# Kernel tuning notes

Hardware: AMD Instinct MI355X
Metric: run time of the kernel (lower is better)

Reference implementation:

```python
import jax, jax.numpy as jnp
import numpy as np
from jax import lax

W_WIN = 7  # window size from init_kwargs


def _dwconv(x, k):
    """Depthwise 2D conv, SAME padding, kernel k: [C,1,kh,kw] (OIHW)."""
    C = x.shape[1]
    p = k.shape[-1] // 2
    return lax.conv_general_dilated(
        x, k, window_strides=(1, 1), padding=[(p, p), (p, p)],
        feature_group_count=C, dimension_numbers=("NCHW", "OIHW", "NCHW"))


def setup_inputs() -> dict:
    key = jax.random.key(0)
    ks = jax.random.split(key, 6)
    B, C, H, Wd = 1, 48, 56, 56
    x = jax.random.normal(ks[0], (B, C, H, Wd), dtype=jnp.float32)
    # small init scale keeps the softmax logits (dot/49) in a sane range
    w3 = jax.random.normal(ks[1], (C, 1, 3, 3), dtype=jnp.float32) * 0.1
    w5 = jax.random.normal(ks[2], (C, 1, 5, 5), dtype=jnp.float32) * 0.1
    w7 = jax.random.normal(ks[3], (C, 1, 7, 7), dtype=jnp.float32) * 0.1
    pw = jax.random.normal(ks[4], (C, 3 * C, 1, 1), dtype=jnp.float32) * 0.05
    pb = jax.random.normal(ks[5], (C,), dtype=jnp.float32) * 0.01
    return {"x": x, "w3": w3, "w5": w5, "w7": w7, "pw": pw, "pb": pb}


def reference(x, w3, w5, w7, pw, pb):
    B, C, H, Wd = x.shape
    w = W_WIN
    # multi-scale depthwise branch, concat on channels -> [B, 3C, H, W]
    y = jnp.concatenate([_dwconv(x, w3), _dwconv(x, w5), _dwconv(x, w7)], axis=1)
    pad_h = (-H) % w
    pad_w = (-Wd) % w
    if pad_h or pad_w:  # static Python ints -> jit-safe
        y = jnp.pad(y, ((0, 0), (0, 0), (0, pad_h), (0, pad_w)), mode="reflect")
    Hp, Wp = y.shape[2], y.shape[3]
    nH, nW = Hp // w, Wp // w
    C3 = 3 * C
    # equivalent to torch unfold(2,w,w).unfold(3,w,w).permute(0,1,2,4,3,5)
    # .reshape(B,3C,nH*nW,w*w): same row-major linearization
    yw = y.reshape(B, C3, nH * nW, w * w)
    # rows: (B, nH*nW, 3C) flattened -> N x (w*w)
    yf = yw.transpose(0, 2, 1, 3).reshape(B * nH * nW * C3, w * w)
    # full N x N self-attention over all rows (faithful to the original)
    attn = jax.nn.softmax((yf @ yf.T) / (w * w), axis=-1)
    y_hat = (attn @ yf).reshape(B, nH, nW, C3, w, w)
    y_hat = y_hat.transpose(0, 3, 1, 4, 2, 5).reshape(B, C3, nH * w, nW * w)
    y_hat = y_hat[:, :, :H, :Wd]
    # 1x1 projection 3C -> C, plus residual
    out = jnp.einsum("oi,bihw->bohw", pw[:, :, 0, 0], y_hat) + pb[None, :, None, None]
    return x + out
```

## Files before the change

kernel.cpp:

```cpp
#include <hip/hip_runtime.h>

typedef unsigned int uint;
typedef unsigned short ushort;
typedef __attribute__((ext_vector_type(8))) short bf16x8;
typedef __attribute__((ext_vector_type(4))) float f32x4;

#define C_IN   48
#define C3     144
#define HW     56
#define SSP    3136
#define DW     49
#define DPAD   64
#define NROWS  9216

#define NSPLIT 12
#define TPS    12

#define CSC 0.02944245f

#define YF_B    0
#define YFT_B   1179648
#define OPART_B 2359296
#define ESUM_B  (OPART_B + NSPLIT * DW * NROWS * 2)


__device__ __forceinline__ ushort f32_to_bf16_rne(float x) {
  uint b = __float_as_uint(x);
  b += 0x7fffu + ((b >> 16) & 1u);
  return (ushort)(b >> 16);
}
__device__ __forceinline__ float bf16_to_f32(ushort u) {
  return __uint_as_float(((uint)u) << 16);
}
__device__ __forceinline__ void async_copy16(const void* g, void* l) {
  __builtin_amdgcn_global_load_lds(
      (const __attribute__((address_space(1))) unsigned int*)g,
      (__attribute__((address_space(3))) unsigned int*)l, 16, 0, 0);
}

__global__ __launch_bounds__(256) void conv_kernel(
    const float* __restrict__ x, const float* __restrict__ w3,
    const float* __restrict__ w5, const float* __restrict__ w7,
    ushort* __restrict__ yf, ushort* __restrict__ yfT) {
  __shared__ ushort tile[4][64];
  const int tid = threadIdx.x;
  const int idx = blockIdx.x * 256 + tid;
  const int r = idx >> 6, t = idx & 63;
  const int rr = r & 3;
  const int r0 = r & ~3;

  ushort ov = 0;
  if (t < DW) {
    int g = r / C3, c3 = r - g * C3;
    int flat = g * DW + t;
    int h = flat / HW, w = flat - h * HW;
    int grp = c3 / C_IN, c = c3 - grp * C_IN;
    const float* wk; int ks;
    if (grp == 0)      { wk = w3 + c * 9;  ks = 3; }
    else if (grp == 1) { wk = w5 + c * 25; ks = 5; }
    else               { wk = w7 + c * 49; ks = 7; }
    int p = ks >> 1;
    const float* xc = x + c * SSP;
    float val = 0.f;
    for (int dy = 0; dy < ks; dy++) {
      int hy = h + dy - p;
      if (hy < 0 || hy >= HW) continue;
      const float* xr = xc + hy * HW;
      const float* wr = wk + dy * ks;
      for (int dx = 0; dx < ks; dx++) {
        int wx = w + dx - p;
        if (wx < 0 || wx >= HW) continue;
        val += xr[wx] * wr[dx];
      }
    }
    ov = f32_to_bf16_rne(val);
  }
  yf[idx] = ov;
  tile[rr][t] = ov;
  __syncthreads();

  if (tid < 64) {
    ushort4 v;
    if (tid == 56) {
      v.x = 0x3F80; v.y = 0x3F80; v.z = 0x3F80; v.w = 0x3F80;
    } else {
      v.x = tile[0][tid]; v.y = tile[1][tid];
      v.z = tile[2][tid]; v.w = tile[3][tid];
    }
    const int k6 = r0 & 63;
    const int pcol = (r0 & ~63) | (k6 & 35) | ((k6 & 12) << 1) | ((k6 & 16) >> 2);
    *(ushort4*)&yfT[tid * NROWS + pcol] = v;
  }
}

__global__ __launch_bounds__(512, 4) void attn_kernel(
    const ushort* __restrict__ yf, const ushort* __restrict__ yfT,
    ushort* __restrict__ opart, float* __restrict__ esum_g) {
  __shared__ __align__(16) char smem[32768];

  const int tid = threadIdx.x;
  const int w = tid >> 6, lane = tid & 63;
  const int q = lane >> 4, c = lane & 15;
  const int m0 = blockIdx.x * 256 + w * 32;
  const int sp = blockIdx.y;

  bf16x8 qf[2][2];
#pragma unroll
  for (int mt = 0; mt < 2; mt++)
#pragma unroll
    for (int ds = 0; ds < 2; ds++) {
      bf16x8 raw = *(const bf16x8*)&yf[(m0 + mt * 16 + c) * 64 + ds * 32 + q * 8];
      short tmp[8];
#pragma unroll
      for (int j = 0; j < 8; j++)
        tmp[j] = (short)f32_to_bf16_rne(bf16_to_f32((ushort)raw[j]) * CSC);
      qf[mt][ds] = *(bf16x8*)tmp;
    }

  f32x4 o[4][2];
#pragma unroll
  for (int dt = 0; dt < 4; dt++)
#pragma unroll
    for (int mt = 0; mt < 2; mt++) o[dt][mt] = (f32x4)0.f;

  {
    const int k0 = (sp * TPS) * 64;
    async_copy16(yf + (k0 + lane) * 64 + w * 8, smem + w * 1024);
    async_copy16(yfT + lane * NROWS + k0 + w * 8, smem + 16384 + w * 1024);
  }
  __syncthreads();

  for (int it = 0; it < TPS; it++) {
    const int cur = it & 1;
    if (it + 1 < TPS) {
      const int k1 = (sp * TPS + it + 1) * 64;
      async_copy16(yf + (k1 + lane) * 64 + w * 8,
                   smem + (cur ^ 1) * 8192 + w * 1024);
      async_copy16(yfT + lane * NROWS + k1 + w * 8,
                   smem + 16384 + (cur ^ 1) * 8192 + w * 1024);
    }

    const char* Kb = smem + cur * 8192;
    const char* Vb = smem + 16384 + cur * 8192;

    bf16x8 bp[2][2];
#pragma unroll
    for (int nc = 0; nc < 2; nc++) {
      f32x4 s[2][2];
#pragma unroll
      for (int h = 0; h < 2; h++) {
        const int nt = nc * 2 + h;
        bf16x8 a0 = *(const bf16x8*)(Kb + q * 1024 + (nt * 16 + c) * 16);
        bf16x8 a1 = *(const bf16x8*)(Kb + (4 + q) * 1024 + (nt * 16 + c) * 16);
#pragma unroll
        for (int mt = 0; mt < 2; mt++) {
          f32x4 acc = (f32x4)0.f;
          acc = __builtin_amdgcn_mfma_f32_16x16x32_bf16(a0, qf[mt][0], acc, 0, 0, 0);
          acc = __builtin_amdgcn_mfma_f32_16x16x32_bf16(a1, qf[mt][1], acc, 0, 0, 0);
          s[h][mt] = acc;
        }
      }
#pragma unroll
      for (int mt = 0; mt < 2; mt++) {
        uint u00 = __float_as_uint(__builtin_amdgcn_exp2f(s[0][mt][0]));
        uint u01 = __float_as_uint(__builtin_amdgcn_exp2f(s[0][mt][1]));
        uint u02 = __float_as_uint(__builtin_amdgcn_exp2f(s[0][mt][2]));
        uint u03 = __float_as_uint(__builtin_amdgcn_exp2f(s[0][mt][3]));
        uint u10 = __float_as_uint(__builtin_amdgcn_exp2f(s[1][mt][0]));
        uint u11 = __float_as_uint(__builtin_amdgcn_exp2f(s[1][mt][1]));
        uint u12 = __float_as_uint(__builtin_amdgcn_exp2f(s[1][mt][2]));
        uint u13 = __float_as_uint(__builtin_amdgcn_exp2f(s[1][mt][3]));
        uint4 t4;
        t4.x = (u00 >> 16) | (u01 & 0xffff0000u);
        t4.y = (u02 >> 16) | (u03 & 0xffff0000u);
        t4.z = (u10 >> 16) | (u11 & 0xffff0000u);
        t4.w = (u12 >> 16) | (u13 & 0xffff0000u);
        bp[mt][nc] = *(bf16x8*)&t4;
      }
    }

#pragma unroll
    for (int dt = 0; dt < 4; dt++) {
      bf16x8 v0 = *(const bf16x8*)(Vb + q * 1024 + (dt * 16 + c) * 16);
      bf16x8 v1 = *(const bf16x8*)(Vb + (4 + q) * 1024 + (dt * 16 + c) * 16);
      o[dt][0] = __builtin_amdgcn_mfma_f32_16x16x32_bf16(v0, bp[0][0], o[dt][0], 0, 0, 0);
      o[dt][1] = __builtin_amdgcn_mfma_f32_16x16x32_bf16(v0, bp[1][0], o[dt][1], 0, 0, 0);
      o[dt][0] = __builtin_amdgcn_mfma_f32_16x16x32_bf16(v1, bp[0][1], o[dt][0], 0, 0, 0);
      o[dt][1] = __builtin_amdgcn_mfma_f32_16x16x32_bf16(v1, bp[1][1], o[dt][1], 0, 0, 0);
    }

    if (it + 1 < TPS) __syncthreads();
  }

#pragma unroll
  for (int dt = 0; dt < 4; dt++)
#pragma unroll
    for (int mt = 0; mt < 2; mt++)
#pragma unroll
      for (int r = 0; r < 4; r++) {
        int d = dt * 16 + q * 4 + r;
        int m = m0 + mt * 16 + c;
        float v = o[dt][mt][r];
        if (d < DW) {
          opart[(sp * DW + d) * NROWS + m] = f32_to_bf16_rne(v);
        } else if (d == 56) {
          esum_g[sp * NROWS + m] = v;
        }
      }
}

__global__ __launch_bounds__(256) void fuse_pw_kernel(
    const ushort* __restrict__ opart, const float* __restrict__ esum_g,
    const float* __restrict__ x, const float* __restrict__ pw,
    const float* __restrict__ pb, float* __restrict__ out) {
  __shared__ float vb[7 * 145];
  __shared__ float inv_es[144];
  const int g = blockIdx.x, tch = blockIdx.y;
  const int t0 = tch * 7;
  const int tid = threadIdx.x;

  if (tid < 144) {
    int r = g * C3 + tid;
    float e = 0.f;
#pragma unroll
    for (int sp = 0; sp < NSPLIT; sp++) e += esum_g[sp * NROWS + r];
    inv_es[tid] = 1.f / e;
  }
  __syncthreads();

  for (int j = tid; j < 7 * 144; j += 256) {
    int tt = j / 144, i = j - tt * 144;
    int r = g * C3 + i, t = t0 + tt;
    float ov = 0.f;
#pragma unroll
    for (int sp = 0; sp < NSPLIT; sp++)
      ov += bf16_to_f32(opart[(sp * DW + t) * NROWS + r]);
    vb[tt * 145 + i] = ov * inv_es[i];
  }
  __syncthreads();

  for (int j = tid; j < C_IN * 7; j += 256) {
    int o = j / 7, tt = j - o * 7;
    int t = t0 + tt;
    const float* pwo = pw + o * C3;
    const float* vrow = &vb[tt * 145];
    float a0 = 0.f, a1 = 0.f, a2 = 0.f, a3 = 0.f;
#pragma unroll
    for (int i = 0; i < C3; i += 4) {
      float4 wv = *(const float4*)&pwo[i];
      a0 += wv.x * vrow[i];
      a1 += wv.y * vrow[i + 1];
      a2 += wv.z * vrow[i + 2];
      a3 += wv.w * vrow[i + 3];
    }
    float acc = (a0 + a1) + (a2 + a3);
    int nh = g >> 3, nw = g & 7;
    int th = t / 7, tw = t - th * 7;
    int oidx = o * SSP + (nh * 7 + th) * HW + (nw * 7 + tw);
    out[oidx] = x[oidx] + pb[o] + acc;
  }
}

extern "C" void kernel_launch(void* const* d_in, const int* in_sizes, int n_in,
                              void* d_out, int out_size, void* d_ws, size_t ws_size,
                              hipStream_t stream) {
  const float* x  = (const float*)d_in[0];
  const float* w3 = (const float*)d_in[1];
  const float* w5 = (const float*)d_in[2];
  const float* w7 = (const float*)d_in[3];
  const float* pw = (const float*)d_in[4];
  const float* pb = (const float*)d_in[5];
  float* out = (float*)d_out;
  char* ws = (char*)d_ws;

  ushort* yf    = (ushort*)(ws + YF_B);
  ushort* yfT   = (ushort*)(ws + YFT_B);
  ushort* opart = (ushort*)(ws + OPART_B);
  float*  esum  = (float*)(ws + ESUM_B);

  conv_kernel<<<(NROWS * DPAD) / 256, 256, 0, stream>>>(x, w3, w5, w7, yf, yfT);
  attn_kernel<<<dim3(NROWS / 256, NSPLIT), 512, 0, stream>>>(yf, yfT, opart, esum);
  fuse_pw_kernel<<<dim3(64, 7), 256, 0, stream>>>(opart, esum, x, pw, pb, out);
}
```

Before: 111.1 us.

## Triple-buffer K/V tiles in attention and vectorize split-reduction loads

The attention kernel moves from double to triple buffering of the K and V tiles in LDS. It prefetches two tiles ahead and uses explicit vmcnt waits with raw barriers instead of __syncthreads, so global loads overlap more compute. The reduction kernel now reads eight bf16 partial outputs per thread with 16-byte vector loads instead of scalar loads. The larger LDS footprint (48KB per block) may reduce occupancy, and the fine-grained waitcnt handling depends on how many loads are outstanding.

Result: no change. 111.2 us (+0.1%).

```diff
diff --git a/kernel.cpp b/kernel.cpp
--- a/kernel.cpp
+++ b/kernel.cpp
@@ -4,6 +4,7 @@
 typedef unsigned short ushort;
 typedef __attribute__((ext_vector_type(8))) short bf16x8;
 typedef __attribute__((ext_vector_type(4))) float f32x4;
+typedef __attribute__((ext_vector_type(8))) unsigned short ushort8v;
 
 #define C_IN   48
 #define C3     144
@@ -96,13 +97,14 @@
 __global__ __launch_bounds__(512, 4) void attn_kernel(
     const ushort* __restrict__ yf, const ushort* __restrict__ yfT,
     ushort* __restrict__ opart, float* __restrict__ esum_g) {
-  __shared__ __align__(16) char smem[32768];
+  __shared__ __align__(16) char smem[49152];
 
   const int tid = threadIdx.x;
   const int w = tid >> 6, lane = tid & 63;
   const int q = lane >> 4, c = lane & 15;
   const int m0 = blockIdx.x * 256 + w * 32;
   const int sp = blockIdx.y;
+  const int base = sp * TPS;
 
   bf16x8 qf[2][2];
 #pragma unroll
@@ -124,24 +126,28 @@
     for (int mt = 0; mt < 2; mt++) o[dt][mt] = (f32x4)0.f;
 
   {
-    const int k0 = (sp * TPS) * 64;
+    const int k0 = base * 64;
     async_copy16(yf + (k0 + lane) * 64 + w * 8, smem + w * 1024);
-    async_copy16(yfT + lane * NROWS + k0 + w * 8, smem + 16384 + w * 1024);
-  }
-  __syncthreads();
+    async_copy16(yfT + lane * NROWS + k0 + w * 8, smem + 24576 + w * 1024);
+    const int k1 = (base + 1) * 64;
+    async_copy16(yf + (k1 + lane) * 64 + w * 8, smem + 8192 + w * 1024);
+    async_copy16(yfT + lane * NROWS + k1 + w * 8, smem + 24576 + 8192 + w * 1024);
+  }
+  asm volatile("s_waitcnt vmcnt(2)" ::: "memory");
+  __builtin_amdgcn_s_barrier();
 
   for (int it = 0; it < TPS; it++) {
-    const int cur = it & 1;
-    if (it + 1 < TPS) {
-      const int k1 = (sp * TPS + it + 1) * 64;
-      async_copy16(yf + (k1 + lane) * 64 + w * 8,
-                   smem + (cur ^ 1) * 8192 + w * 1024);
-      async_copy16(yfT + lane * NROWS + k1 + w * 8,
-                   smem + 16384 + (cur ^ 1) * 8192 + w * 1024);
-    }
-
-    const char* Kb = smem + cur * 8192;
-    const char* Vb = smem + 16384 + cur * 8192;
+    const int buf = it % 3;
+    if (it + 2 < TPS) {
+      const int bn = (it + 2) % 3;
+      const int kn = (base + it + 2) * 64;
+      async_copy16(yf + (kn + lane) * 64 + w * 8, smem + bn * 8192 + w * 1024);
+      async_copy16(yfT + lane * NROWS + kn + w * 8,
+                   smem + 24576 + bn * 8192 + w * 1024);
+    }
+
+    const char* Kb = smem + buf * 8192;
+    const char* Vb = smem + 24576 + buf * 8192;
 
     bf16x8 bp[2][2];
 #pragma unroll
@@ -189,7 +195,11 @@
       o[dt][1] = __builtin_amdgcn_mfma_f32_16x16x32_bf16(v1, bp[1][1], o[dt][1], 0, 0, 0);
     }
 
-    if (it + 1 < TPS) __syncthreads();
+    if (it + 1 < TPS) {
+      if (it + 2 < TPS) asm volatile("s_waitcnt vmcnt(2)" ::: "memory");
+      else              asm volatile("s_waitcnt vmcnt(0)" ::: "memory");
+      __builtin_amdgcn_s_barrier();
+    }
   }
 
 #pragma unroll
@@ -228,14 +238,22 @@
   }
   __syncthreads();
 
-  for (int j = tid; j < 7 * 144; j += 256) {
-    int tt = j / 144, i = j - tt * 144;
-    int r = g * C3 + i, t = t0 + tt;
-    float ov = 0.f;
-#pragma unroll
-    for (int sp = 0; sp < NSPLIT; sp++)
-      ov += bf16_to_f32(opart[(sp * DW + t) * NROWS + r]);
-    vb[tt * 145 + i] = ov * inv_es[i];
+  for (int j = tid; j < 7 * 18; j += 256) {
+    int tt = j / 18, ch = j - tt * 18;
+    int i0 = ch * 8;
+    int t = t0 + tt;
+    float acc[8];
+#pragma unroll
+    for (int k = 0; k < 8; k++) acc[k] = 0.f;
+#pragma unroll
+    for (int sp = 0; sp < NSPLIT; sp++) {
+      ushort8v v = *(const ushort8v*)&opart[(sp * DW + t) * NROWS + g * C3 + i0];
+#pragma unroll
+      for (int k = 0; k < 8; k++) acc[k] += bf16_to_f32(v[k]);
+    }
+#pragma unroll
+    for (int k = 0; k < 8; k++)
+      vb[tt * 145 + i0 + k] = acc[k] * inv_es[i0 + k];
   }
   __syncthreads();
 
```
